# Kernel optimization log

Measured on AMD Instinct MI355X. Metric: run time of the kernel, lower is better.

## Reference

```python
import jax, jax.numpy as jnp
import numpy as np

N = 50000
EPS = 1e-5


def gcn_conv(x, edge_index, W, b):
    # x: [N, Fin] -> [N, Fout]; symmetric-normalized aggregation with self-loops
    h = x @ W  # [N, Fout]
    src = jnp.concatenate([edge_index[0], jnp.arange(N, dtype=edge_index.dtype)])
    dst = jnp.concatenate([edge_index[1], jnp.arange(N, dtype=edge_index.dtype)])
    deg = jax.ops.segment_sum(jnp.ones_like(dst, dtype=h.dtype), dst, num_segments=N)
    dinv = jnp.where(deg > 0, jax.lax.rsqrt(deg), 0.0)
    norm = dinv[src] * dinv[dst]  # [E+N]
    msg = h[src] * norm[:, None]  # [E+N, Fout]
    out = jax.ops.segment_sum(msg, dst, num_segments=N)
    return out + b


def batch_norm_eval(x, gamma, beta, mean, var):
    return (x - mean) * jax.lax.rsqrt(var + EPS) * gamma + beta


def setup_inputs() -> dict:
    key = jax.random.key(0)
    ks = jax.random.split(key, 16)
    Fin, H, C = 128, 64, 40
    inp = {
        "x": jax.random.normal(ks[0], (N, Fin), dtype=jnp.float32),
        "edge_index": jax.random.randint(ks[1], (2, 1600000), 0, N, dtype=jnp.int64),
        "W1": jax.random.normal(ks[2], (Fin, H), dtype=jnp.float32) / np.sqrt(Fin),
        "b1": jnp.zeros((H,), jnp.float32),
        "g1": jax.random.normal(ks[3], (H,), jnp.float32) * 0.1 + 1.0,
        "be1": jax.random.normal(ks[4], (H,), jnp.float32) * 0.1,
        "m1": jax.random.normal(ks[5], (H,), jnp.float32) * 0.1,
        "v1": jax.random.uniform(ks[6], (H,), jnp.float32, 0.5, 1.5),
        "W2": jax.random.normal(ks[7], (H, H), dtype=jnp.float32) / np.sqrt(H),
        "b2": jnp.zeros((H,), jnp.float32),
        "g2": jax.random.normal(ks[8], (H,), jnp.float32) * 0.1 + 1.0,
        "be2": jax.random.normal(ks[9], (H,), jnp.float32) * 0.1,
        "m2": jax.random.normal(ks[10], (H,), jnp.float32) * 0.1,
        "v2": jax.random.uniform(ks[11], (H,), jnp.float32, 0.5, 1.5),
        "W3": jax.random.normal(ks[12], (H, C), dtype=jnp.float32) / np.sqrt(H),
        "b3": jnp.zeros((C,), jnp.float32),
    }
    return inp


def reference(x, edge_index, W1, b1, g1, be1, m1, v1, W2, b2, g2, be2, m2, v2, W3, b3):
    # eval-mode forward: dropout is identity, BatchNorm uses running stats
    h = gcn_conv(x, edge_index, W1, b1)
    h = jax.nn.relu(batch_norm_eval(h, g1, be1, m1, v1))
    h = gcn_conv(h, edge_index, W2, b2)
    h = jax.nn.relu(batch_norm_eval(h, g2, be2, m2, v2))
    return gcn_conv(h, edge_index, W3, b3)
```

## Files before the change

kernel.cpp:

```cpp
#include <hip/hip_runtime.h>
#include <hip/hip_fp16.h>

#define BN_EPS 1e-5f

typedef _Float16 half2_t __attribute__((ext_vector_type(2)));
typedef _Float16 half8_t __attribute__((ext_vector_type(8)));

static __device__ __forceinline__ float fdot2(half2_t a, half2_t b, float c) {
    return __builtin_amdgcn_fdot2(a, b, c, false);
}


__global__ void k_zero(int* __restrict__ p, int n) {
    int i = threadIdx.x;
    if (i < n) p[i] = 0;
}

__global__ void k_bcount(const int* __restrict__ dst, int* __restrict__ btot, int E, int B) {
    __shared__ int cnt[256];
    int tid = threadIdx.x;
    cnt[tid] = 0;
    __syncthreads();
    int e0 = blockIdx.x * 2048;
#pragma unroll
    for (int j = 0; j < 8; ++j) {
        int e = e0 + j * 256 + tid;
        if (e < E) atomicAdd(&cnt[dst[e] >> 8], 1);
    }
    __syncthreads();
    if (tid < B && cnt[tid] > 0) atomicAdd(&btot[tid], cnt[tid]);
}

__global__ void k_bscan(const int* __restrict__ btot, int* __restrict__ bbase,
                        int* __restrict__ bcur, int* __restrict__ row_ptr, int N, int B) {
    __shared__ int sc[256];
    int tid = threadIdx.x;
    int v = (tid < B) ? btot[tid] : 0;
    sc[tid] = v;
    __syncthreads();
    for (int off = 1; off < 256; off <<= 1) {
        int t = (tid >= off) ? sc[tid - off] : 0;
        __syncthreads();
        sc[tid] += t;
        __syncthreads();
    }
    int excl = sc[tid] - v;
    if (tid < B) { bbase[tid] = excl; bcur[tid] = excl; }
    if (tid == B - 1) { bbase[B] = excl + v; row_ptr[N] = excl + v; }
}

__global__ void k_bscatter(const int* __restrict__ src, const int* __restrict__ dst,
                           int* bcur, unsigned int* __restrict__ ebuf, int E, int B) {
    __shared__ int cnt[256];
    __shared__ int gb[256];
    int tid = threadIdx.x;
    cnt[tid] = 0;
    __syncthreads();
    int e0 = blockIdx.x * 2048;
    int bk[8], rk[8];
    unsigned int pay[8];
#pragma unroll
    for (int j = 0; j < 8; ++j) {
        int e = e0 + j * 256 + tid;
        if (e < E) {
            int d = dst[e];
            int b = d >> 8;
            bk[j] = b;
            rk[j] = atomicAdd(&cnt[b], 1);
            pay[j] = (unsigned int)src[e] | ((unsigned int)(d & 255) << 16);
        } else {
            bk[j] = -1; rk[j] = 0; pay[j] = 0;
        }
    }
    __syncthreads();
    if (tid < B && cnt[tid] > 0) gb[tid] = atomicAdd(&bcur[tid], cnt[tid]);
    __syncthreads();
#pragma unroll
    for (int j = 0; j < 8; ++j)
        if (bk[j] >= 0) ebuf[gb[bk[j]] + rk[j]] = pay[j];
}

__global__ void k_bfinal(const unsigned int* __restrict__ ebuf, const int* __restrict__ bbase,
                         int* __restrict__ row_ptr, float* __restrict__ dinv,
                         unsigned short* __restrict__ col, int N) {
    __shared__ int cnt[256];
    __shared__ int sc[256];
    __shared__ int cur[256];
    int tid = threadIdx.x;
    int b = blockIdx.x;
    int node0 = b << 8;
    int ebeg = bbase[b], eend = bbase[b + 1];

    cnt[tid] = 0;
    __syncthreads();
    for (int i = ebeg + tid; i < eend; i += 256)
        atomicAdd(&cnt[ebuf[i] >> 16], 1);
    __syncthreads();
    int myc = cnt[tid];
    sc[tid] = myc;
    __syncthreads();
    for (int off = 1; off < 256; off <<= 1) {
        int t = (tid >= off) ? sc[tid - off] : 0;
        __syncthreads();
        sc[tid] += t;
        __syncthreads();
    }
    int excl = sc[tid] - myc;
    cur[tid] = ebeg + excl;
    int node = node0 + tid;
    if (node < N) {
        row_ptr[node] = ebeg + excl;
        dinv[node] = rsqrtf((float)(myc + 1));
    }
    __syncthreads();
    for (int i = ebeg + tid; i < eend; i += 256) {
        unsigned int p = ebuf[i];
        int dl = p >> 16;
        int pos = atomicAdd(&cur[dl], 1);
        col[pos] = (unsigned short)(p & 0xFFFFu);
    }
}

template <int K, int FOUT, bool FP16IN>
__launch_bounds__(256)
__global__ void k_gemm_scale(const void* __restrict__ Xv, const float* __restrict__ W,
                             const float* __restrict__ dinv, half2_t* __restrict__ HS, int N) {
    constexpr int KK = K / 2;
    constexpr int XSTR = (K == 128) ? 66 : 36;
    __shared__ half2_t xs2[64][XSTR];
    __shared__ half2_t wl2[KK][FOUT];
    int tid = threadIdx.x;
    int row0 = blockIdx.x * 64;

    if constexpr (FP16IN) {
        const _Float16* X = (const _Float16*)Xv;
        constexpr int U = 64 * K / 8;
        for (int u = tid; u < U; u += 256) {
            int row = u / (K / 8), q = u % (K / 8);
            int grow = row0 + row;
            uint4 v = make_uint4(0u, 0u, 0u, 0u);
            if (grow < N) v = *(const uint4*)&X[(size_t)grow * K + q * 8];
            *(uint4*)&xs2[row][q * 4] = v;
        }
    } else {
        const float* X = (const float*)Xv;
        constexpr int U = 64 * K / 4;
        for (int u = tid; u < U; u += 256) {
            int row = u / (K / 4), c = u % (K / 4);
            int grow = row0 + row;
            half2_t h0 = (half2_t)(_Float16)0, h1 = (half2_t)(_Float16)0;
            if (grow < N) {
                float4 v = *(const float4*)&X[(size_t)grow * K + c * 4];
                h0[0] = (_Float16)v.x; h0[1] = (_Float16)v.y;
                h1[0] = (_Float16)v.z; h1[1] = (_Float16)v.w;
            }
            xs2[row][2 * c] = h0;
            xs2[row][2 * c + 1] = h1;
        }
    }
    for (int i = tid; i < KK * FOUT; i += 256) {
        int kk = i / FOUT, f = i % FOUT;
        half2_t h;
        h[0] = (_Float16)W[(2 * kk) * FOUT + f];
        h[1] = (_Float16)W[(2 * kk + 1) * FOUT + f];
        wl2[kk][f] = h;
    }
    __syncthreads();

    int tc = tid & 15, tr = tid >> 4;
    if (4 * tc < FOUT) {
        float acc[4][4] = {};
#pragma unroll 4
        for (int kk = 0; kk < KK; ++kk) {
            half2_t a0 = xs2[4 * tr + 0][kk];
            half2_t a1 = xs2[4 * tr + 1][kk];
            half2_t a2 = xs2[4 * tr + 2][kk];
            half2_t a3 = xs2[4 * tr + 3][kk];
            half8_t wv = *(const half8_t*)&wl2[kk][4 * tc];
            half2_t w0 = {wv[0], wv[1]};
            half2_t w1 = {wv[2], wv[3]};
            half2_t w2 = {wv[4], wv[5]};
            half2_t w3 = {wv[6], wv[7]};
            acc[0][0] = fdot2(a0, w0, acc[0][0]); acc[0][1] = fdot2(a0, w1, acc[0][1]);
            acc[0][2] = fdot2(a0, w2, acc[0][2]); acc[0][3] = fdot2(a0, w3, acc[0][3]);
            acc[1][0] = fdot2(a1, w0, acc[1][0]); acc[1][1] = fdot2(a1, w1, acc[1][1]);
            acc[1][2] = fdot2(a1, w2, acc[1][2]); acc[1][3] = fdot2(a1, w3, acc[1][3]);
            acc[2][0] = fdot2(a2, w0, acc[2][0]); acc[2][1] = fdot2(a2, w1, acc[2][1]);
            acc[2][2] = fdot2(a2, w2, acc[2][2]); acc[2][3] = fdot2(a2, w3, acc[2][3]);
            acc[3][0] = fdot2(a3, w0, acc[3][0]); acc[3][1] = fdot2(a3, w1, acc[3][1]);
            acc[3][2] = fdot2(a3, w2, acc[3][2]); acc[3][3] = fdot2(a3, w3, acc[3][3]);
        }
#pragma unroll
        for (int i = 0; i < 4; ++i) {
            int row = row0 + 4 * tr + i;
            if (row < N) {
                float dv = dinv[row];
                half2_t p0, p1;
                p0[0] = (_Float16)(dv * acc[i][0]); p0[1] = (_Float16)(dv * acc[i][1]);
                p1[0] = (_Float16)(dv * acc[i][2]); p1[1] = (_Float16)(dv * acc[i][3]);
                HS[(size_t)row * (FOUT / 2) + 2 * tc] = p0;
                HS[(size_t)row * (FOUT / 2) + 2 * tc + 1] = p1;
            }
        }
    }
}

template <int FOUT, bool BN>
__launch_bounds__(256)
__global__ void k_agg(const half8_t* __restrict__ hs8, const unsigned short* __restrict__ col,
                      const int* __restrict__ row_ptr, const float* __restrict__ dinv,
                      const float* __restrict__ b, const float* __restrict__ g,
                      const float* __restrict__ be, const float* __restrict__ m,
                      const float* __restrict__ v, void* __restrict__ outv, int N) {
    constexpr int NS = FOUT / 8;
    int gtid = blockIdx.x * blockDim.x + threadIdx.x;
    int wave = gtid >> 6;
    int lane = gtid & 63;
    int g8 = lane >> 3;
    int s = lane & 7;
    int nwaves = (gridDim.x * blockDim.x) >> 6;
    bool act = s < NS;

    float bias[8], sf[8], tf[8];
    if (act) {
#pragma unroll
        for (int j = 0; j < 8; ++j) {
            int f = 8 * s + j;
            bias[j] = b[f];
            if (BN) {
                sf[j] = g[f] * rsqrtf(v[f] + BN_EPS);
                tf[j] = be[f] - m[f] * sf[j];
            }
        }
    }

    for (int node = wave; node < N; node += nwaves) {
        int beg = row_ptr[node], end = row_ptr[node + 1];
        float acc0[8] = {}, acc1[8] = {};
        if (act && g8 == 0) {
            half8_t t = hs8[(size_t)node * NS + s];
#pragma unroll
            for (int j = 0; j < 8; ++j) acc0[j] = (float)t[j];
        }
        int e = beg + g8;
        for (; e + 8 < end; e += 16) {
            int i0 = col[e];
            int i1 = col[e + 8];
            if (act) {
                half8_t t0 = hs8[(size_t)i0 * NS + s];
                half8_t t1 = hs8[(size_t)i1 * NS + s];
#pragma unroll
                for (int j = 0; j < 8; ++j) { acc0[j] += (float)t0[j]; acc1[j] += (float)t1[j]; }
            }
        }
        if (e < end) {
            int i0 = col[e];
            if (act) {
                half8_t t0 = hs8[(size_t)i0 * NS + s];
#pragma unroll
                for (int j = 0; j < 8; ++j) acc0[j] += (float)t0[j];
            }
        }
#pragma unroll
        for (int j = 0; j < 8; ++j) {
            float sj = acc0[j] + acc1[j];
            sj += __shfl_xor(sj, 8);
            sj += __shfl_xor(sj, 16);
            sj += __shfl_xor(sj, 32);
            acc0[j] = sj;
        }
        if (g8 == 0 && act) {
            float dv = dinv[node];
            if (BN) {
                half8_t h;
#pragma unroll
                for (int j = 0; j < 8; ++j) {
                    float o = dv * acc0[j] + bias[j];
                    o = fmaxf(o * sf[j] + tf[j], 0.0f);
                    h[j] = (_Float16)o;
                }
                ((half8_t*)outv)[(size_t)node * NS + s] = h;
            } else {
                float o[8];
#pragma unroll
                for (int j = 0; j < 8; ++j) o[j] = dv * acc0[j] + bias[j];
                float* op = (float*)outv + (size_t)node * FOUT + 8 * s;
                *(float4*)op = make_float4(o[0], o[1], o[2], o[3]);
                *(float4*)(op + 4) = make_float4(o[4], o[5], o[6], o[7]);
            }
        }
    }
}


extern "C" void kernel_launch(void* const* d_in, const int* in_sizes, int n_in,
                              void* d_out, int out_size, void* d_ws, size_t ws_size,
                              hipStream_t stream) {
    const float* x   = (const float*)d_in[0];
    const int*   ei  = (const int*)d_in[1];
    const float* W1  = (const float*)d_in[2];
    const float* b1  = (const float*)d_in[3];
    const float* g1  = (const float*)d_in[4];
    const float* be1 = (const float*)d_in[5];
    const float* m1  = (const float*)d_in[6];
    const float* v1  = (const float*)d_in[7];
    const float* W2  = (const float*)d_in[8];
    const float* b2  = (const float*)d_in[9];
    const float* g2  = (const float*)d_in[10];
    const float* be2 = (const float*)d_in[11];
    const float* m2  = (const float*)d_in[12];
    const float* v2  = (const float*)d_in[13];
    const float* W3  = (const float*)d_in[14];
    const float* b3  = (const float*)d_in[15];

    const int FIN = 128, H = 64;
    int N = in_sizes[0] / FIN;
    int E = in_sizes[1] / 2;
    const int* src = ei;
    const int* dst = ei + E;
    int B = (N + 255) >> 8;

    char* ws = (char*)d_ws;
    size_t off = 0;
    auto carve = [&](size_t bytes) -> void* {
        void* p = ws + off;
        off += (bytes + 255) & ~(size_t)255;
        return p;
    };
    float*  dinv    = (float*)carve((size_t)N * 4);
    int*    row_ptr = (int*)carve((size_t)(N + 1) * 4);
    unsigned short* col = (unsigned short*)carve((size_t)E * 2);
    unsigned int*   ebuf = (unsigned int*)carve((size_t)E * 4);
    half2_t* hs     = (half2_t*)carve((size_t)N * H * 2);
    _Float16* y     = (_Float16*)carve((size_t)N * H * 2);
    int*    btot    = (int*)carve(512 * 4);
    int*    bbase   = (int*)carve(512 * 4);
    int*    bcur    = (int*)carve(512 * 4);
    (void)ws_size; (void)n_in; (void)out_size;

    int eb2k = (E + 2047) / 2048;

    k_zero<<<1, 256, 0, stream>>>(btot, B);
    k_bcount<<<eb2k, 256, 0, stream>>>(dst, btot, E, B);
    k_bscan<<<1, 256, 0, stream>>>(btot, bbase, bcur, row_ptr, N, B);
    k_bscatter<<<eb2k, 256, 0, stream>>>(src, dst, bcur, ebuf, E, B);
    k_bfinal<<<B, 256, 0, stream>>>(ebuf, bbase, row_ptr, dinv, col, N);

    int gb = (N + 63) / 64;
    const half8_t* hs8 = (const half8_t*)hs;
    k_gemm_scale<128, 64, false><<<gb, 256, 0, stream>>>(x, W1, dinv, hs, N);
    k_agg<64, true><<<4096, 256, 0, stream>>>(hs8, col, row_ptr, dinv, b1, g1, be1, m1, v1, y, N);
    k_gemm_scale<64, 64, true><<<gb, 256, 0, stream>>>(y, W2, dinv, hs, N);
    k_agg<64, true><<<4096, 256, 0, stream>>>(hs8, col, row_ptr, dinv, b2, g2, be2, m2, v2, y, N);
    k_gemm_scale<64, 40, true><<<gb, 256, 0, stream>>>(y, W3, dinv, hs, N);
    k_agg<40, false><<<4096, 256, 0, stream>>>(hs8, col, row_ptr, dinv, b3, nullptr, nullptr, nullptr, nullptr,
                                               d_out, N);
}
```

Measured before the change: 220.9 us.

## Split hidden features into two 32-wide planes for cache-friendlier aggregation

The 64-wide fp16 hidden features are stored as two separate 32-wide planes. Each GCN aggregation now runs as two passes, one per plane, so each pass gathers randomly from a table half the size, which fits L2 better. The GEMM kernel now reads and writes the split planes. The aggregation kernel is generalised so four lanes serve one node's features and sixteen edges are in flight per wave. Column-index loads become nontemporal. The cost is reading the CSR structure twice and running extra kernel launches.

```diff
diff --git a/kernel.cpp b/kernel.cpp
--- a/kernel.cpp
+++ b/kernel.cpp
@@ -123,8 +123,9 @@
 
 template <int K, int FOUT, bool FP16IN>
 __launch_bounds__(256)
-__global__ void k_gemm_scale(const void* __restrict__ Xv, const float* __restrict__ W,
-                             const float* __restrict__ dinv, half2_t* __restrict__ HS, int N) {
+__global__ void k_gemm_scale(const void* __restrict__ XAv, const void* __restrict__ XBv,
+                             const float* __restrict__ W, const float* __restrict__ dinv,
+                             half2_t* __restrict__ HA, half2_t* __restrict__ HB, int N) {
     constexpr int KK = K / 2;
     constexpr int XSTR = (K == 128) ? 66 : 36;
     __shared__ half2_t xs2[64][XSTR];
@@ -133,17 +134,22 @@
     int row0 = blockIdx.x * 64;
 
     if constexpr (FP16IN) {
-        const _Float16* X = (const _Float16*)Xv;
-        constexpr int U = 64 * K / 8;
+        const _Float16* XA = (const _Float16*)XAv;
+        const _Float16* XB = (const _Float16*)XBv;
+        constexpr int U = 64 * 8;
         for (int u = tid; u < U; u += 256) {
-            int row = u / (K / 8), q = u % (K / 8);
+            int row = u >> 3, q = u & 7;
             int grow = row0 + row;
             uint4 v = make_uint4(0u, 0u, 0u, 0u);
-            if (grow < N) v = *(const uint4*)&X[(size_t)grow * K + q * 8];
+            if (grow < N) {
+                const _Float16* p = (q < 4) ? &XA[(size_t)grow * 32 + q * 8]
+                                            : &XB[(size_t)grow * 32 + (q - 4) * 8];
+                v = *(const uint4*)p;
+            }
             *(uint4*)&xs2[row][q * 4] = v;
         }
     } else {
-        const float* X = (const float*)Xv;
+        const float* X = (const float*)XAv;
         constexpr int U = 64 * K / 4;
         for (int u = tid; u < U; u += 256) {
             int row = u / (K / 4), c = u % (K / 4);
@@ -198,8 +204,15 @@
                 half2_t p0, p1;
                 p0[0] = (_Float16)(dv * acc[i][0]); p0[1] = (_Float16)(dv * acc[i][1]);
                 p1[0] = (_Float16)(dv * acc[i][2]); p1[1] = (_Float16)(dv * acc[i][3]);
-                HS[(size_t)row * (FOUT / 2) + 2 * tc] = p0;
-                HS[(size_t)row * (FOUT / 2) + 2 * tc + 1] = p1;
+                if constexpr (FOUT == 64) {
+                    half2_t* plane = (tc < 8) ? HA : HB;
+                    int o = (tc & 7) * 2;
+                    plane[(size_t)row * 16 + o] = p0;
+                    plane[(size_t)row * 16 + o + 1] = p1;
+                } else {
+                    HA[(size_t)row * (FOUT / 2) + 2 * tc] = p0;
+                    HA[(size_t)row * (FOUT / 2) + 2 * tc + 1] = p1;
+                }
             }
         }
     }
@@ -213,11 +226,13 @@
                       const float* __restrict__ be, const float* __restrict__ m,
                       const float* __restrict__ v, void* __restrict__ outv, int N) {
     constexpr int NS = FOUT / 8;
+    constexpr int GL = (FOUT <= 32) ? 4 : 8;
+    constexpr int NG = 64 / GL;
     int gtid = blockIdx.x * blockDim.x + threadIdx.x;
     int wave = gtid >> 6;
     int lane = gtid & 63;
-    int g8 = lane >> 3;
-    int s = lane & 7;
+    int g8 = lane / GL;
+    int s = lane % GL;
     int nwaves = (gridDim.x * blockDim.x) >> 6;
     bool act = s < NS;
 
@@ -243,9 +258,9 @@
             for (int j = 0; j < 8; ++j) acc0[j] = (float)t[j];
         }
         int e = beg + g8;
-        for (; e + 8 < end; e += 16) {
-            int i0 = col[e];
-            int i1 = col[e + 8];
+        for (; e + NG < end; e += 2 * NG) {
+            int i0 = __builtin_nontemporal_load(&col[e]);
+            int i1 = __builtin_nontemporal_load(&col[e + NG]);
             if (act) {
                 half8_t t0 = hs8[(size_t)i0 * NS + s];
                 half8_t t1 = hs8[(size_t)i1 * NS + s];
@@ -254,7 +269,7 @@
             }
         }
         if (e < end) {
-            int i0 = col[e];
+            int i0 = __builtin_nontemporal_load(&col[e]);
             if (act) {
                 half8_t t0 = hs8[(size_t)i0 * NS + s];
 #pragma unroll
@@ -264,9 +279,8 @@
 #pragma unroll
         for (int j = 0; j < 8; ++j) {
             float sj = acc0[j] + acc1[j];
-            sj += __shfl_xor(sj, 8);
-            sj += __shfl_xor(sj, 16);
-            sj += __shfl_xor(sj, 32);
+#pragma unroll
+            for (int off = GL; off < 64; off <<= 1) sj += __shfl_xor(sj, off);
             acc0[j] = sj;
         }
         if (g8 == 0 && act) {
@@ -331,8 +345,11 @@
     int*    row_ptr = (int*)carve((size_t)(N + 1) * 4);
     unsigned short* col = (unsigned short*)carve((size_t)E * 2);
     unsigned int*   ebuf = (unsigned int*)carve((size_t)E * 4);
-    half2_t* hs     = (half2_t*)carve((size_t)N * H * 2);
-    _Float16* y     = (_Float16*)carve((size_t)N * H * 2);
+    half2_t* hsA    = (half2_t*)carve((size_t)N * 32 * 2);
+    half2_t* hsB    = (half2_t*)carve((size_t)N * 32 * 2);
+    half2_t* yA     = (half2_t*)carve((size_t)N * 32 * 2);
+    half2_t* yB     = (half2_t*)carve((size_t)N * 32 * 2);
+    half2_t* hs40   = (half2_t*)carve((size_t)N * 40 * 2);
     int*    btot    = (int*)carve(512 * 4);
     int*    bbase   = (int*)carve(512 * 4);
     int*    bcur    = (int*)carve(512 * 4);
@@ -347,12 +364,17 @@
     k_bfinal<<<B, 256, 0, stream>>>(ebuf, bbase, row_ptr, dinv, col, N);
 
     int gb = (N + 63) / 64;
-    const half8_t* hs8 = (const half8_t*)hs;
-    k_gemm_scale<128, 64, false><<<gb, 256, 0, stream>>>(x, W1, dinv, hs, N);
-    k_agg<64, true><<<4096, 256, 0, stream>>>(hs8, col, row_ptr, dinv, b1, g1, be1, m1, v1, y, N);
-    k_gemm_scale<64, 64, true><<<gb, 256, 0, stream>>>(y, W2, dinv, hs, N);
-    k_agg<64, true><<<4096, 256, 0, stream>>>(hs8, col, row_ptr, dinv, b2, g2, be2, m2, v2, y, N);
-    k_gemm_scale<64, 40, true><<<gb, 256, 0, stream>>>(y, W3, dinv, hs, N);
-    k_agg<40, false><<<4096, 256, 0, stream>>>(hs8, col, row_ptr, dinv, b3, nullptr, nullptr, nullptr, nullptr,
-                                               d_out, N);
-}
+    k_gemm_scale<128, 64, false><<<gb, 256, 0, stream>>>(x, nullptr, W1, dinv, hsA, hsB, N);
+    k_agg<32, true><<<4096, 256, 0, stream>>>((const half8_t*)hsA, col, row_ptr, dinv,
+                                              b1, g1, be1, m1, v1, yA, N);
+    k_agg<32, true><<<4096, 256, 0, stream>>>((const half8_t*)hsB, col, row_ptr, dinv,
+                                              b1 + 32, g1 + 32, be1 + 32, m1 + 32, v1 + 32, yB, N);
+    k_gemm_scale<64, 64, true><<<gb, 256, 0, stream>>>(yA, yB, W2, dinv, hsA, hsB, N);
+    k_agg<32, true><<<4096, 256, 0, stream>>>((const half8_t*)hsA, col, row_ptr, dinv,
+                                              b2, g2, be2, m2, v2, yA, N);
+    k_agg<32, true><<<4096, 256, 0, stream>>>((const half8_t*)hsB, col, row_ptr, dinv,
+                                              b2 + 32, g2 + 32, be2 + 32, m2 + 32, v2 + 32, yB, N);
+    k_gemm_scale<64, 40, true><<<gb, 256, 0, stream>>>(yA, yB, W3, dinv, hs40, nullptr, N);
+    k_agg<40, false><<<4096, 256, 0, stream>>>((const half8_t*)hs40, col, row_ptr, dinv,
+                                               b3, nullptr, nullptr, nullptr, nullptr, d_out, N);
+}
```

After: 278.3 us. +26.0%, slower.

## Split aggregation into two source-half passes for cache locality

Applied to the files above, without the earlier changes.

The CSR build now sorts each row's neighbors into two groups, sources below N/2 and sources at or above N/2, and records a row_mid pointer. Each aggregation becomes two kernels. The first gathers only from the lower half of the feature table and writes fp32 partial sums. The second gathers from the upper half, adds the partials, and applies bias, BN and ReLU. The aim is to halve the gather working set so it fits better in cache, at the cost of an extra launch plus a write and read of an N×F fp32 partial buffer per layer. It also adds nontemporal loads for col and for the partials.

```diff
diff --git a/kernel.cpp b/kernel.cpp
--- a/kernel.cpp
+++ b/kernel.cpp
@@ -5,6 +5,7 @@
 
 typedef _Float16 half2_t __attribute__((ext_vector_type(2)));
 typedef _Float16 half8_t __attribute__((ext_vector_type(8)));
+typedef float f32x4 __attribute__((ext_vector_type(4)));
 
 static __device__ __forceinline__ float fdot2(half2_t a, half2_t b, float c) {
     return __builtin_amdgcn_fdot2(a, b, c, false);
@@ -81,22 +82,31 @@
 }
 
 __global__ void k_bfinal(const unsigned int* __restrict__ ebuf, const int* __restrict__ bbase,
-                         int* __restrict__ row_ptr, float* __restrict__ dinv,
-                         unsigned short* __restrict__ col, int N) {
+                         int* __restrict__ row_ptr, int* __restrict__ row_mid,
+                         float* __restrict__ dinv, unsigned short* __restrict__ col,
+                         int N, int HN) {
     __shared__ int cnt[256];
+    __shared__ int cntA[256];
     __shared__ int sc[256];
-    __shared__ int cur[256];
+    __shared__ int curA[256];
+    __shared__ int curB[256];
     int tid = threadIdx.x;
     int b = blockIdx.x;
     int node0 = b << 8;
     int ebeg = bbase[b], eend = bbase[b + 1];
 
     cnt[tid] = 0;
-    __syncthreads();
-    for (int i = ebeg + tid; i < eend; i += 256)
-        atomicAdd(&cnt[ebuf[i] >> 16], 1);
+    cntA[tid] = 0;
+    __syncthreads();
+    for (int i = ebeg + tid; i < eend; i += 256) {
+        unsigned int p = ebuf[i];
+        int dl = p >> 16;
+        atomicAdd(&cnt[dl], 1);
+        if ((int)(p & 0xFFFFu) < HN) atomicAdd(&cntA[dl], 1);
+    }
     __syncthreads();
     int myc = cnt[tid];
+    int mya = cntA[tid];
     sc[tid] = myc;
     __syncthreads();
     for (int off = 1; off < 256; off <<= 1) {
@@ -106,18 +116,22 @@
         __syncthreads();
     }
     int excl = sc[tid] - myc;
-    cur[tid] = ebeg + excl;
+    int base = ebeg + excl;
+    curA[tid] = base;
+    curB[tid] = base + mya;
     int node = node0 + tid;
     if (node < N) {
-        row_ptr[node] = ebeg + excl;
+        row_ptr[node] = base;
+        row_mid[node] = base + mya;
         dinv[node] = rsqrtf((float)(myc + 1));
     }
     __syncthreads();
     for (int i = ebeg + tid; i < eend; i += 256) {
         unsigned int p = ebuf[i];
         int dl = p >> 16;
-        int pos = atomicAdd(&cur[dl], 1);
-        col[pos] = (unsigned short)(p & 0xFFFFu);
+        int s = (int)(p & 0xFFFFu);
+        int pos = (s < HN) ? atomicAdd(&curA[dl], 1) : atomicAdd(&curB[dl], 1);
+        col[pos] = (unsigned short)s;
     }
 }
 
@@ -205,14 +219,14 @@
     }
 }
 
-template <int FOUT, bool BN>
+
+template <int FOUT>
 __launch_bounds__(256)
-__global__ void k_agg(const half8_t* __restrict__ hs8, const unsigned short* __restrict__ col,
-                      const int* __restrict__ row_ptr, const float* __restrict__ dinv,
-                      const float* __restrict__ b, const float* __restrict__ g,
-                      const float* __restrict__ be, const float* __restrict__ m,
-                      const float* __restrict__ v, void* __restrict__ outv, int N) {
+__global__ void k_aggA(const half8_t* __restrict__ hs8, const unsigned short* __restrict__ col,
+                       const int* __restrict__ row_ptr, const int* __restrict__ row_mid,
+                       float* __restrict__ partial, int N) {
     constexpr int NS = FOUT / 8;
+    constexpr int NG = 8;
     int gtid = blockIdx.x * blockDim.x + threadIdx.x;
     int wave = gtid >> 6;
     int lane = gtid & 63;
@@ -221,6 +235,64 @@
     int nwaves = (gridDim.x * blockDim.x) >> 6;
     bool act = s < NS;
 
+    for (int node = wave; node < N; node += nwaves) {
+        int beg = row_ptr[node], end = row_mid[node];
+        float acc0[8] = {}, acc1[8] = {};
+        int e = beg + g8;
+        for (; e + NG < end; e += 2 * NG) {
+            int i0 = __builtin_nontemporal_load(&col[e]);
+            int i1 = __builtin_nontemporal_load(&col[e + NG]);
+            if (act) {
+                half8_t t0 = hs8[(size_t)i0 * NS + s];
+                half8_t t1 = hs8[(size_t)i1 * NS + s];
+#pragma unroll
+                for (int j = 0; j < 8; ++j) { acc0[j] += (float)t0[j]; acc1[j] += (float)t1[j]; }
+            }
+        }
+        if (e < end) {
+            int i0 = __builtin_nontemporal_load(&col[e]);
+            if (act) {
+                half8_t t0 = hs8[(size_t)i0 * NS + s];
+#pragma unroll
+                for (int j = 0; j < 8; ++j) acc0[j] += (float)t0[j];
+            }
+        }
+#pragma unroll
+        for (int j = 0; j < 8; ++j) {
+            float sj = acc0[j] + acc1[j];
+            sj += __shfl_xor(sj, 8);
+            sj += __shfl_xor(sj, 16);
+            sj += __shfl_xor(sj, 32);
+            acc0[j] = sj;
+        }
+        if (g8 == 0 && act) {
+            float* op = partial + (size_t)node * FOUT + 8 * s;
+            f32x4 v0 = {acc0[0], acc0[1], acc0[2], acc0[3]};
+            f32x4 v1 = {acc0[4], acc0[5], acc0[6], acc0[7]};
+            __builtin_nontemporal_store(v0, (f32x4*)op);
+            __builtin_nontemporal_store(v1, (f32x4*)(op + 4));
+        }
+    }
+}
+
+template <int FOUT, bool BN>
+__launch_bounds__(256)
+__global__ void k_aggB(const half8_t* __restrict__ hs8, const unsigned short* __restrict__ col,
+                       const int* __restrict__ row_ptr, const int* __restrict__ row_mid,
+                       const float* __restrict__ partial, const float* __restrict__ dinv,
+                       const float* __restrict__ b, const float* __restrict__ g,
+                       const float* __restrict__ be, const float* __restrict__ m,
+                       const float* __restrict__ v, void* __restrict__ outv, int N) {
+    constexpr int NS = FOUT / 8;
+    constexpr int NG = 8;
+    int gtid = blockIdx.x * blockDim.x + threadIdx.x;
+    int wave = gtid >> 6;
+    int lane = gtid & 63;
+    int g8 = lane >> 3;
+    int s = lane & 7;
+    int nwaves = (gridDim.x * blockDim.x) >> 6;
+    bool act = s < NS;
+
     float bias[8], sf[8], tf[8];
     if (act) {
 #pragma unroll
@@ -235,7 +307,7 @@
     }
 
     for (int node = wave; node < N; node += nwaves) {
-        int beg = row_ptr[node], end = row_ptr[node + 1];
+        int beg = row_mid[node], end = row_ptr[node + 1];
         float acc0[8] = {}, acc1[8] = {};
         if (act && g8 == 0) {
             half8_t t = hs8[(size_t)node * NS + s];
@@ -243,9 +315,9 @@
             for (int j = 0; j < 8; ++j) acc0[j] = (float)t[j];
         }
         int e = beg + g8;
-        for (; e + 8 < end; e += 16) {
-            int i0 = col[e];
-            int i1 = col[e + 8];
+        for (; e + NG < end; e += 2 * NG) {
+            int i0 = __builtin_nontemporal_load(&col[e]);
+            int i1 = __builtin_nontemporal_load(&col[e + NG]);
             if (act) {
                 half8_t t0 = hs8[(size_t)i0 * NS + s];
                 half8_t t1 = hs8[(size_t)i1 * NS + s];
@@ -254,7 +326,7 @@
             }
         }
         if (e < end) {
-            int i0 = col[e];
+            int i0 = __builtin_nontemporal_load(&col[e]);
             if (act) {
                 half8_t t0 = hs8[(size_t)i0 * NS + s];
 #pragma unroll
@@ -270,12 +342,17 @@
             acc0[j] = sj;
         }
         if (g8 == 0 && act) {
+            const float* pp = partial + (size_t)node * FOUT + 8 * s;
+            f32x4 p0 = __builtin_nontemporal_load((const f32x4*)pp);
+            f32x4 p1 = __builtin_nontemporal_load((const f32x4*)(pp + 4));
+            float tot[8] = {acc0[0] + p0[0], acc0[1] + p0[1], acc0[2] + p0[2], acc0[3] + p0[3],
+                            acc0[4] + p1[0], acc0[5] + p1[1], acc0[6] + p1[2], acc0[7] + p1[3]};
             float dv = dinv[node];
             if (BN) {
                 half8_t h;
 #pragma unroll
                 for (int j = 0; j < 8; ++j) {
-                    float o = dv * acc0[j] + bias[j];
+                    float o = dv * tot[j] + bias[j];
                     o = fmaxf(o * sf[j] + tf[j], 0.0f);
                     h[j] = (_Float16)o;
                 }
@@ -283,7 +360,7 @@
             } else {
                 float o[8];
 #pragma unroll
-                for (int j = 0; j < 8; ++j) o[j] = dv * acc0[j] + bias[j];
+                for (int j = 0; j < 8; ++j) o[j] = dv * tot[j] + bias[j];
                 float* op = (float*)outv + (size_t)node * FOUT + 8 * s;
                 *(float4*)op = make_float4(o[0], o[1], o[2], o[3]);
                 *(float4*)(op + 4) = make_float4(o[4], o[5], o[6], o[7]);
@@ -319,6 +396,7 @@
     const int* src = ei;
     const int* dst = ei + E;
     int B = (N + 255) >> 8;
+    int HN = N / 2;
 
     char* ws = (char*)d_ws;
     size_t off = 0;
@@ -329,10 +407,12 @@
     };
     float*  dinv    = (float*)carve((size_t)N * 4);
     int*    row_ptr = (int*)carve((size_t)(N + 1) * 4);
+    int*    row_mid = (int*)carve((size_t)N * 4);
     unsigned short* col = (unsigned short*)carve((size_t)E * 2);
     unsigned int*   ebuf = (unsigned int*)carve((size_t)E * 4);
     half2_t* hs     = (half2_t*)carve((size_t)N * H * 2);
     _Float16* y     = (_Float16*)carve((size_t)N * H * 2);
+    float*  part    = (float*)carve((size_t)N * H * 4);
     int*    btot    = (int*)carve(512 * 4);
     int*    bbase   = (int*)carve(512 * 4);
     int*    bcur    = (int*)carve(512 * 4);
@@ -344,15 +424,21 @@
     k_bcount<<<eb2k, 256, 0, stream>>>(dst, btot, E, B);
     k_bscan<<<1, 256, 0, stream>>>(btot, bbase, bcur, row_ptr, N, B);
     k_bscatter<<<eb2k, 256, 0, stream>>>(src, dst, bcur, ebuf, E, B);
-    k_bfinal<<<B, 256, 0, stream>>>(ebuf, bbase, row_ptr, dinv, col, N);
+    k_bfinal<<<B, 256, 0, stream>>>(ebuf, bbase, row_ptr, row_mid, dinv, col, N, HN);
 
     int gb = (N + 63) / 64;
     const half8_t* hs8 = (const half8_t*)hs;
     k_gemm_scale<128, 64, false><<<gb, 256, 0, stream>>>(x, W1, dinv, hs, N);
-    k_agg<64, true><<<4096, 256, 0, stream>>>(hs8, col, row_ptr, dinv, b1, g1, be1, m1, v1, y, N);
+    k_aggA<64><<<4096, 256, 0, stream>>>(hs8, col, row_ptr, row_mid, part, N);
+    k_aggB<64, true><<<4096, 256, 0, stream>>>(hs8, col, row_ptr, row_mid, part, dinv,
+                                               b1, g1, be1, m1, v1, y, N);
     k_gemm_scale<64, 64, true><<<gb, 256, 0, stream>>>(y, W2, dinv, hs, N);
-    k_agg<64, true><<<4096, 256, 0, stream>>>(hs8, col, row_ptr, dinv, b2, g2, be2, m2, v2, y, N);
+    k_aggA<64><<<4096, 256, 0, stream>>>(hs8, col, row_ptr, row_mid, part, N);
+    k_aggB<64, true><<<4096, 256, 0, stream>>>(hs8, col, row_ptr, row_mid, part, dinv,
+                                               b2, g2, be2, m2, v2, y, N);
     k_gemm_scale<64, 40, true><<<gb, 256, 0, stream>>>(y, W3, dinv, hs, N);
-    k_agg<40, false><<<4096, 256, 0, stream>>>(hs8, col, row_ptr, dinv, b3, nullptr, nullptr, nullptr, nullptr,
-                                               d_out, N);
-}
+    k_aggA<40><<<4096, 256, 0, stream>>>(hs8, col, row_ptr, row_mid, (float*)d_out, N);
+    k_aggB<40, false><<<4096, 256, 0, stream>>>(hs8, col, row_ptr, row_mid, (const float*)d_out,
+                                                dinv, b3, nullptr, nullptr, nullptr, nullptr,
+                                                d_out, N);
+}
```

New measurement: 282.1 us. 1.28x slower.
